# Kernel tuning notes

Hardware: AMD Instinct MI355X
Metric: run time of the kernel (lower is better)

Reference implementation:

```python
import jax, jax.numpy as jnp
import numpy as np

B, K, C, O, I = 32, 1024, 64, 32, 32  # batch, num_capsules, num_classes, out_dim, in_dim
NUM_ROUTING = 3


def squash(x, axis=-1):
    sq = jnp.sum(x * x, axis=axis, keepdims=True)
    return (sq / (1.0 + sq)) * x / jnp.sqrt(sq + 1e-8)


def setup_inputs() -> dict:
    key = jax.random.key(0)
    kx, kw = jax.random.split(key)
    x = jax.random.normal(kx, (B, K, I), dtype=jnp.float32)
    W = jax.random.normal(kw, (K, C, O, I), dtype=jnp.float32) * 0.01
    return {"x": x, "W": W}


def reference(x, W):
    # u_hat[b,k,c,o] = sum_i W[k,c,o,i] * x[b,k,i]  (the torch repeat+matmul)
    u_hat = jnp.einsum('kcoi,bki->bkco', W, x)  # [B,K,C,O]
    b_ij = jnp.zeros((B, K, C, 1), dtype=x.dtype)
    c_ij = None
    v_j = None
    for i in range(NUM_ROUTING):
        c_ij = jax.nn.softmax(b_ij, axis=2)              # softmax over classes
        s_j = jnp.sum(c_ij * u_hat, axis=1, keepdims=True)  # [B,1,C,O]
        v_j = squash(s_j, axis=-1)
        if i < NUM_ROUTING - 1:
            agreement = jnp.sum(u_hat * v_j, axis=-1, keepdims=True)  # [B,K,C,1]
            b_ij = b_ij + agreement
    return v_j[:, 0], c_ij[..., 0]  # ([B,C,O], [B,K,C])
```

## Files before the change

kernel.cpp:

```cpp
#include <hip/hip_runtime.h>
#include <stdint.h>

#define Bb 32
#define Kk 1024
#define Cc 64
#define Oo 32
#define Ii 32

typedef __attribute__((ext_vector_type(8))) short bf16x8;
typedef __attribute__((ext_vector_type(4))) float f32x4;

__device__ __forceinline__ short f2bf(float f) {
    uint32_t u = __builtin_bit_cast(uint32_t, f);
    u += 0x7fffu + ((u >> 16) & 1u);
    return (short)(u >> 16);
}
__device__ __forceinline__ float bflo(uint32_t u) { return __builtin_bit_cast(float, u << 16); }
__device__ __forceinline__ float bfhi(uint32_t u) { return __builtin_bit_cast(float, u & 0xffff0000u); }
__device__ __forceinline__ uint32_t pk2(float a, float b) {
    return (uint32_t)(uint16_t)f2bf(a) | ((uint32_t)(uint16_t)f2bf(b) << 16);
}


__global__ __launch_bounds__(256) void k_uhat(const float* __restrict__ x,
                                              const float* __restrict__ W,
                                              uint32_t* __restrict__ uh) {
    const int k = blockIdx.x;
    const int lane = threadIdx.x & 63;
    const int wave = threadIdx.x >> 6;
    const int m = lane & 15;
    const int q = lane >> 4;

    bf16x8 bfrag[2];
#pragma unroll
    for (int nb = 0; nb < 2; ++nb) {
        const float* xp = x + (size_t)((nb * 16 + m) * Kk + k) * Ii + q * 8;
        f32x4 a = *(const f32x4*)xp;
        f32x4 b = *(const f32x4*)(xp + 4);
        bf16x8 t;
        t[0] = f2bf(a.x); t[1] = f2bf(a.y); t[2] = f2bf(a.z); t[3] = f2bf(a.w);
        t[4] = f2bf(b.x); t[5] = f2bf(b.y); t[6] = f2bf(b.z); t[7] = f2bf(b.w);
        bfrag[nb] = t;
    }

    for (int cc = 0; cc < 16; ++cc) {
        const int c = wave * 16 + cc;
        bf16x8 afrag[2];
#pragma unroll
        for (int mo = 0; mo < 2; ++mo) {
            const float* wp = W + (size_t)((k * Cc + c) * Oo + mo * 16 + m) * Ii + q * 8;
            f32x4 a = __builtin_nontemporal_load((const f32x4*)wp);
            f32x4 b = __builtin_nontemporal_load((const f32x4*)(wp + 4));
            bf16x8 t;
            t[0] = f2bf(a.x); t[1] = f2bf(a.y); t[2] = f2bf(a.z); t[3] = f2bf(a.w);
            t[4] = f2bf(b.x); t[5] = f2bf(b.y); t[6] = f2bf(b.z); t[7] = f2bf(b.w);
            afrag[mo] = t;
        }
        const f32x4 z = {0.f, 0.f, 0.f, 0.f};
        f32x4 d0 = __builtin_amdgcn_mfma_f32_16x16x32_bf16(afrag[0], bfrag[0], z, 0, 0, 0);
        f32x4 d1 = __builtin_amdgcn_mfma_f32_16x16x32_bf16(afrag[0], bfrag[1], z, 0, 0, 0);
        f32x4 d2 = __builtin_amdgcn_mfma_f32_16x16x32_bf16(afrag[1], bfrag[0], z, 0, 0, 0);
        f32x4 d3 = __builtin_amdgcn_mfma_f32_16x16x32_bf16(afrag[1], bfrag[1], z, 0, 0, 0);

        uint4 p0, p1;
        p0.x = pk2(d0.x, d0.y); p0.y = pk2(d0.z, d0.w);
        p0.z = pk2(d1.x, d1.y); p0.w = pk2(d1.z, d1.w);
        p1.x = pk2(d2.x, d2.y); p1.y = pk2(d2.z, d2.w);
        p1.z = pk2(d3.x, d3.y); p1.w = pk2(d3.z, d3.w);
        uint32_t* dst = uh + (size_t)(k * Cc + c) * 512 + lane * 4;
        *(uint4*)dst = p0;
        *(uint4*)(dst + 256) = p1;
    }
}

template <bool UNIFORM>
__global__ __launch_bounds__(256) void k_sacc(const uint32_t* __restrict__ uh,
                                              const float* __restrict__ cij,
                                              float* __restrict__ part) {
    const int lane = threadIdx.x & 63;
    const int wave = threadIdx.x >> 6;
    const int m = lane & 15;
    const int c = (blockIdx.x & 15) * 4 + wave;
    const int chunk = blockIdx.x >> 4;
    const int k0 = chunk * 32;

    float acc[16];
#pragma unroll
    for (int i = 0; i < 16; ++i) acc[i] = 0.f;

    for (int kl = 0; kl < 32; ++kl) {
        const int k = k0 + kl;
        const uint32_t* up = uh + (size_t)(k * Cc + c) * 512 + lane * 4;
        uint4 q0 = *(const uint4*)up;
        uint4 q1 = *(const uint4*)(up + 256);
        float w0, w1;
        if (UNIFORM) {
            w0 = w1 = 1.0f / 64.0f;
        } else {
            const float* cp = cij + (size_t)(k * Cc + c) * Bb + m;
            w0 = cp[0];
            w1 = cp[16];
        }
        acc[0]  += w0 * bflo(q0.x);  acc[1]  += w0 * bfhi(q0.x);
        acc[2]  += w0 * bflo(q0.y);  acc[3]  += w0 * bfhi(q0.y);
        acc[4]  += w1 * bflo(q0.z);  acc[5]  += w1 * bfhi(q0.z);
        acc[6]  += w1 * bflo(q0.w);  acc[7]  += w1 * bfhi(q0.w);
        acc[8]  += w0 * bflo(q1.x);  acc[9]  += w0 * bfhi(q1.x);
        acc[10] += w0 * bflo(q1.y);  acc[11] += w0 * bfhi(q1.y);
        acc[12] += w1 * bflo(q1.z);  acc[13] += w1 * bfhi(q1.z);
        acc[14] += w1 * bflo(q1.w);  acc[15] += w1 * bfhi(q1.w);
    }
#pragma unroll
    for (int t = 0; t < 4; ++t) {
        f32x4 v = {acc[t * 4 + 0], acc[t * 4 + 1], acc[t * 4 + 2], acc[t * 4 + 3]};
        *(f32x4*)&part[(((size_t)(chunk * Cc + c) * 4 + t) * 64 + lane) * 4] = v;
    }
}

template <bool FINAL>
__global__ __launch_bounds__(256) void k_reduce(const float* __restrict__ part,
                                                float* __restrict__ vfrag,
                                                float* __restrict__ out_v) {
    __shared__ float red[4 * 64 * 17];
    const int c = blockIdx.x;
    const int tid = threadIdx.x;
    const int lane = tid & 63;
    const int cg = tid >> 6;

    float acc[16];
#pragma unroll
    for (int i = 0; i < 16; ++i) acc[i] = 0.f;
    for (int ch = cg * 8; ch < cg * 8 + 8; ++ch) {
        const f32x4* p = (const f32x4*)part + (size_t)(ch * Cc + c) * 4 * 64 + lane;
#pragma unroll
        for (int t = 0; t < 4; ++t) {
            f32x4 v = p[t * 64];
            acc[t * 4 + 0] += v.x; acc[t * 4 + 1] += v.y;
            acc[t * 4 + 2] += v.z; acc[t * 4 + 3] += v.w;
        }
    }
#pragma unroll
    for (int i = 0; i < 16; ++i) red[(cg * 64 + lane) * 17 + i] = acc[i];
    __syncthreads();

    if (tid < 64) {
        float a[16];
#pragma unroll
        for (int i = 0; i < 16; ++i)
            a[i] = red[tid * 17 + i] + red[(64 + tid) * 17 + i]
                 + red[(128 + tid) * 17 + i] + red[(192 + tid) * 17 + i];
        float sq0 = 0.f, sq1 = 0.f;
#pragma unroll
        for (int r = 0; r < 4; ++r) {
            sq0 += a[r] * a[r] + a[8 + r] * a[8 + r];
            sq1 += a[4 + r] * a[4 + r] + a[12 + r] * a[12 + r];
        }
        sq0 += __shfl_xor(sq0, 16); sq0 += __shfl_xor(sq0, 32);
        sq1 += __shfl_xor(sq1, 16); sq1 += __shfl_xor(sq1, 32);
        const float c0 = sq0 / ((1.f + sq0) * sqrtf(sq0 + 1e-8f));
        const float c1 = sq1 / ((1.f + sq1) * sqrtf(sq1 + 1e-8f));
#pragma unroll
        for (int r = 0; r < 4; ++r) {
            a[r] *= c0; a[8 + r] *= c0;
            a[4 + r] *= c1; a[12 + r] *= c1;
        }
        float* vp = vfrag + ((size_t)c * 64 + tid) * 16;
#pragma unroll
        for (int t = 0; t < 4; ++t) {
            f32x4 v = {a[t * 4 + 0], a[t * 4 + 1], a[t * 4 + 2], a[t * 4 + 3]};
            *(f32x4*)(vp + t * 4) = v;
        }
        if (FINAL) {
            const int m = tid & 15, q = tid >> 4;
#pragma unroll
            for (int t = 0; t < 4; ++t)
#pragma unroll
                for (int r = 0; r < 4; ++r) {
                    const int b = (t & 1) * 16 + m;
                    const int o = (t >> 1) * 16 + q * 4 + r;
                    out_v[((size_t)b * Cc + c) * Oo + o] = a[t * 4 + r];
                }
        }
    }
}

template <bool FIRST>
__global__ __launch_bounds__(256) void k_route(const uint32_t* __restrict__ uh,
                                               const float* __restrict__ vfrag,
                                               float* __restrict__ bbuf,
                                               float* __restrict__ cbuf,
                                               float* __restrict__ outc) {
    __shared__ float agr[4 * 64 * 32];
    const int tid = threadIdx.x;
    const int lane = tid & 63;
    const int wave = tid >> 6;
    const int m = lane & 15;
    const int q = lane >> 4;
    const int k0 = blockIdx.x * 4;

    for (int cc = 0; cc < 16; ++cc) {
        const int c = wave * 16 + cc;
        const float* vp = vfrag + ((size_t)c * 64 + lane) * 16;
        f32x4 vv[4];
#pragma unroll
        for (int t = 0; t < 4; ++t) vv[t] = *(const f32x4*)(vp + t * 4);
#pragma unroll
        for (int kl = 0; kl < 4; ++kl) {
            const int k = k0 + kl;
            const uint32_t* up = uh + (size_t)(k * Cc + c) * 512 + lane * 4;
            uint4 q0 = *(const uint4*)up;
            uint4 q1 = *(const uint4*)(up + 256);
            float p0 = bflo(q0.x) * vv[0].x + bfhi(q0.x) * vv[0].y
                     + bflo(q0.y) * vv[0].z + bfhi(q0.y) * vv[0].w
                     + bflo(q1.x) * vv[2].x + bfhi(q1.x) * vv[2].y
                     + bflo(q1.y) * vv[2].z + bfhi(q1.y) * vv[2].w;
            float p1 = bflo(q0.z) * vv[1].x + bfhi(q0.z) * vv[1].y
                     + bflo(q0.w) * vv[1].z + bfhi(q0.w) * vv[1].w
                     + bflo(q1.z) * vv[3].x + bfhi(q1.z) * vv[3].y
                     + bflo(q1.w) * vv[3].z + bfhi(q1.w) * vv[3].w;
            p0 += __shfl_xor(p0, 16);
            p0 += __shfl_xor(p0, 32);
            p1 += __shfl_xor(p1, 16);
            p1 += __shfl_xor(p1, 32);
            if (q == 0) {
                agr[(kl * 64 + c) * 32 + m] = p0;
                agr[(kl * 64 + c) * 32 + 16 + m] = p1;
            }
        }
    }
    __syncthreads();

    if (tid < 128) {
        const int kl = tid >> 5;
        const int b = tid & 31;
        const int k = k0 + kl;
        float row[64];
#pragma unroll
        for (int c = 0; c < 64; ++c) row[c] = agr[(kl * 64 + c) * 32 + b];
        if (FIRST) {
            float* bp = bbuf + (size_t)(k * Bb + b) * Cc;
#pragma unroll
            for (int c = 0; c < 64; ++c) bp[c] = row[c];
        } else {
            const float* bp = bbuf + (size_t)(k * Bb + b) * Cc;
#pragma unroll
            for (int c = 0; c < 64; ++c) row[c] += bp[c];
        }
        float mx = row[0];
#pragma unroll
        for (int c = 1; c < 64; ++c) mx = fmaxf(mx, row[c]);
        float sum = 0.f;
#pragma unroll
        for (int c = 0; c < 64; ++c) { row[c] = __expf(row[c] - mx); sum += row[c]; }
        const float inv = 1.f / sum;
#pragma unroll
        for (int c = 0; c < 64; ++c) row[c] *= inv;
        if (!FIRST) {
            float* op = outc + (size_t)(b * Kk + k) * Cc;
#pragma unroll
            for (int c = 0; c < 64; ++c) op[c] = row[c];
        }
#pragma unroll
        for (int c = 0; c < 64; ++c) agr[(kl * 64 + c) * 32 + b] = row[c];
    }
    __syncthreads();

    for (int idx = tid; idx < 4 * 64 * 32; idx += 256) {
        const int kl = idx >> 11;
        const int rem = idx & 2047;
        const int c = rem >> 5;
        const int b = rem & 31;
        cbuf[((size_t)(k0 + kl) * Cc + c) * Bb + b] = agr[idx];
    }
}

extern "C" void kernel_launch(void* const* d_in, const int* in_sizes, int n_in,
                              void* d_out, int out_size, void* d_ws, size_t ws_size,
                              hipStream_t stream) {
    (void)in_sizes; (void)n_in; (void)out_size;
    const float* x = (const float*)d_in[0];
    const float* W = (const float*)d_in[1];
    float* out_v = (float*)d_out;
    float* out_c = out_v + Bb * Cc * Oo;

    char* ws = (char*)d_ws;
    const size_t UH_BYTES = (size_t)Kk * Cc * 512 * 4;
    const size_t PART_BYTES = (size_t)32 * Cc * 4 * 64 * 4 * 4;
    const size_t BB_BYTES = (size_t)Kk * Bb * Cc * 4;
    const size_t VF_BYTES = (size_t)Cc * 64 * 16 * 4;

    uint32_t* uh = (uint32_t*)ws;
    float* part  = (float*)(ws + UH_BYTES);
    float* bbuf  = (float*)(ws + UH_BYTES + PART_BYTES);
    float* cbuf  = (float*)(ws + UH_BYTES + PART_BYTES + BB_BYTES);
    float* vfrag = (float*)(ws + UH_BYTES + PART_BYTES + 2 * BB_BYTES);
    const size_t NEED = UH_BYTES + PART_BYTES + 2 * BB_BYTES + VF_BYTES;
    if (ws_size < NEED) return;

    k_uhat<<<Kk, 256, 0, stream>>>(x, W, uh);
    k_sacc<true><<<512, 256, 0, stream>>>(uh, nullptr, part);
    k_reduce<false><<<Cc, 256, 0, stream>>>(part, vfrag, nullptr);
    k_route<true><<<256, 256, 0, stream>>>(uh, vfrag, bbuf, cbuf, nullptr);
    k_sacc<false><<<512, 256, 0, stream>>>(uh, cbuf, part);
    k_reduce<false><<<Cc, 256, 0, stream>>>(part, vfrag, nullptr);
    k_route<false><<<256, 256, 0, stream>>>(uh, vfrag, bbuf, cbuf, out_c);
    k_sacc<false><<<512, 256, 0, stream>>>(uh, cbuf, part);
    k_reduce<true><<<Cc, 256, 0, stream>>>(part, vfrag, out_v);
}
```

Measured before the change: 519.0 us.

## Fuse routing softmax with weighted s_j accumulation and split reduction in two stages

The routing kernel now also computes the c_ij-weighted partial sums of u_hat for its 4 capsules, reading the softmax weights from shared memory. This removes the cbuf round trip and the separate k_sacc pass over u_hat. Partials are stored as bf16 and reduced in two stages (k_red1 over 512 blocks, then k_red2 per class), which gives more parallelism than the old 64-block reduce. Blocks grow to 512 threads. The trade-off is extra precision loss from bf16 partials and more kernel launches.

```diff
diff --git a/kernel.cpp b/kernel.cpp
--- a/kernel.cpp
+++ b/kernel.cpp
@@ -73,13 +73,10 @@
     }
 }
 
-template <bool UNIFORM>
-__global__ __launch_bounds__(256) void k_sacc(const uint32_t* __restrict__ uh,
-                                              const float* __restrict__ cij,
-                                              float* __restrict__ part) {
+__global__ __launch_bounds__(256) void k_sacc0(const uint32_t* __restrict__ uh,
+                                               float* __restrict__ part0) {
     const int lane = threadIdx.x & 63;
     const int wave = threadIdx.x >> 6;
-    const int m = lane & 15;
     const int c = (blockIdx.x & 15) * 4 + wave;
     const int chunk = blockIdx.x >> 4;
     const int k0 = chunk * 32;
@@ -89,38 +86,28 @@
     for (int i = 0; i < 16; ++i) acc[i] = 0.f;
 
     for (int kl = 0; kl < 32; ++kl) {
-        const int k = k0 + kl;
-        const uint32_t* up = uh + (size_t)(k * Cc + c) * 512 + lane * 4;
+        const uint32_t* up = uh + (size_t)((k0 + kl) * Cc + c) * 512 + lane * 4;
         uint4 q0 = *(const uint4*)up;
         uint4 q1 = *(const uint4*)(up + 256);
-        float w0, w1;
-        if (UNIFORM) {
-            w0 = w1 = 1.0f / 64.0f;
-        } else {
-            const float* cp = cij + (size_t)(k * Cc + c) * Bb + m;
-            w0 = cp[0];
-            w1 = cp[16];
-        }
+        const float w0 = 1.0f / 64.0f;
         acc[0]  += w0 * bflo(q0.x);  acc[1]  += w0 * bfhi(q0.x);
         acc[2]  += w0 * bflo(q0.y);  acc[3]  += w0 * bfhi(q0.y);
-        acc[4]  += w1 * bflo(q0.z);  acc[5]  += w1 * bfhi(q0.z);
-        acc[6]  += w1 * bflo(q0.w);  acc[7]  += w1 * bfhi(q0.w);
+        acc[4]  += w0 * bflo(q0.z);  acc[5]  += w0 * bfhi(q0.z);
+        acc[6]  += w0 * bflo(q0.w);  acc[7]  += w0 * bfhi(q0.w);
         acc[8]  += w0 * bflo(q1.x);  acc[9]  += w0 * bfhi(q1.x);
         acc[10] += w0 * bflo(q1.y);  acc[11] += w0 * bfhi(q1.y);
-        acc[12] += w1 * bflo(q1.z);  acc[13] += w1 * bfhi(q1.z);
-        acc[14] += w1 * bflo(q1.w);  acc[15] += w1 * bfhi(q1.w);
+        acc[12] += w0 * bflo(q1.z);  acc[13] += w0 * bfhi(q1.z);
+        acc[14] += w0 * bflo(q1.w);  acc[15] += w0 * bfhi(q1.w);
     }
 #pragma unroll
     for (int t = 0; t < 4; ++t) {
         f32x4 v = {acc[t * 4 + 0], acc[t * 4 + 1], acc[t * 4 + 2], acc[t * 4 + 3]};
-        *(f32x4*)&part[(((size_t)(chunk * Cc + c) * 4 + t) * 64 + lane) * 4] = v;
-    }
-}
-
-template <bool FINAL>
-__global__ __launch_bounds__(256) void k_reduce(const float* __restrict__ part,
-                                                float* __restrict__ vfrag,
-                                                float* __restrict__ out_v) {
+        *(f32x4*)&part0[(((size_t)(chunk * Cc + c) * 4 + t) * 64 + lane) * 4] = v;
+    }
+}
+
+__global__ __launch_bounds__(256) void k_reduce0(const float* __restrict__ part0,
+                                                 float* __restrict__ vfrag) {
     __shared__ float red[4 * 64 * 17];
     const int c = blockIdx.x;
     const int tid = threadIdx.x;
@@ -131,7 +118,7 @@
 #pragma unroll
     for (int i = 0; i < 16; ++i) acc[i] = 0.f;
     for (int ch = cg * 8; ch < cg * 8 + 8; ++ch) {
-        const f32x4* p = (const f32x4*)part + (size_t)(ch * Cc + c) * 4 * 64 + lane;
+        const f32x4* p = (const f32x4*)part0 + (size_t)(ch * Cc + c) * 4 * 64 + lane;
 #pragma unroll
         for (int t = 0; t < 4; ++t) {
             f32x4 v = p[t * 64];
@@ -170,54 +157,43 @@
             f32x4 v = {a[t * 4 + 0], a[t * 4 + 1], a[t * 4 + 2], a[t * 4 + 3]};
             *(f32x4*)(vp + t * 4) = v;
         }
-        if (FINAL) {
-            const int m = tid & 15, q = tid >> 4;
-#pragma unroll
-            for (int t = 0; t < 4; ++t)
-#pragma unroll
-                for (int r = 0; r < 4; ++r) {
-                    const int b = (t & 1) * 16 + m;
-                    const int o = (t >> 1) * 16 + q * 4 + r;
-                    out_v[((size_t)b * Cc + c) * Oo + o] = a[t * 4 + r];
-                }
-        }
-    }
-}
-
-template <bool FIRST>
-__global__ __launch_bounds__(256) void k_route(const uint32_t* __restrict__ uh,
-                                               const float* __restrict__ vfrag,
-                                               float* __restrict__ bbuf,
-                                               float* __restrict__ cbuf,
-                                               float* __restrict__ outc) {
+    }
+}
+
+template <bool FINAL>
+__global__ __launch_bounds__(512) void k_iter(const uint32_t* __restrict__ uh,
+                                              const float* __restrict__ vfrag,
+                                              float* __restrict__ bbuf,
+                                              uint32_t* __restrict__ partB,
+                                              float* __restrict__ outc) {
     __shared__ float agr[4 * 64 * 32];
     const int tid = threadIdx.x;
     const int lane = tid & 63;
-    const int wave = tid >> 6;
+    const int w = tid >> 6;
     const int m = lane & 15;
     const int q = lane >> 4;
     const int k0 = blockIdx.x * 4;
 
-    for (int cc = 0; cc < 16; ++cc) {
-        const int c = wave * 16 + cc;
+    for (int cc = 0; cc < 8; ++cc) {
+        const int c = w * 8 + cc;
         const float* vp = vfrag + ((size_t)c * 64 + lane) * 16;
-        f32x4 vv[4];
-#pragma unroll
-        for (int t = 0; t < 4; ++t) vv[t] = *(const f32x4*)(vp + t * 4);
+        f32x4 vv0 = *(const f32x4*)(vp);
+        f32x4 vv1 = *(const f32x4*)(vp + 4);
+        f32x4 vv2 = *(const f32x4*)(vp + 8);
+        f32x4 vv3 = *(const f32x4*)(vp + 12);
 #pragma unroll
         for (int kl = 0; kl < 4; ++kl) {
-            const int k = k0 + kl;
-            const uint32_t* up = uh + (size_t)(k * Cc + c) * 512 + lane * 4;
+            const uint32_t* up = uh + (size_t)((k0 + kl) * Cc + c) * 512 + lane * 4;
             uint4 q0 = *(const uint4*)up;
             uint4 q1 = *(const uint4*)(up + 256);
-            float p0 = bflo(q0.x) * vv[0].x + bfhi(q0.x) * vv[0].y
-                     + bflo(q0.y) * vv[0].z + bfhi(q0.y) * vv[0].w
-                     + bflo(q1.x) * vv[2].x + bfhi(q1.x) * vv[2].y
-                     + bflo(q1.y) * vv[2].z + bfhi(q1.y) * vv[2].w;
-            float p1 = bflo(q0.z) * vv[1].x + bfhi(q0.z) * vv[1].y
-                     + bflo(q0.w) * vv[1].z + bfhi(q0.w) * vv[1].w
-                     + bflo(q1.z) * vv[3].x + bfhi(q1.z) * vv[3].y
-                     + bflo(q1.w) * vv[3].z + bfhi(q1.w) * vv[3].w;
+            float p0 = bflo(q0.x) * vv0.x + bfhi(q0.x) * vv0.y
+                     + bflo(q0.y) * vv0.z + bfhi(q0.y) * vv0.w
+                     + bflo(q1.x) * vv2.x + bfhi(q1.x) * vv2.y
+                     + bflo(q1.y) * vv2.z + bfhi(q1.y) * vv2.w;
+            float p1 = bflo(q0.z) * vv1.x + bfhi(q0.z) * vv1.y
+                     + bflo(q0.w) * vv1.z + bfhi(q0.w) * vv1.w
+                     + bflo(q1.z) * vv3.x + bfhi(q1.z) * vv3.y
+                     + bflo(q1.w) * vv3.z + bfhi(q1.w) * vv3.w;
             p0 += __shfl_xor(p0, 16);
             p0 += __shfl_xor(p0, 32);
             p1 += __shfl_xor(p1, 16);
@@ -237,7 +213,7 @@
         float row[64];
 #pragma unroll
         for (int c = 0; c < 64; ++c) row[c] = agr[(kl * 64 + c) * 32 + b];
-        if (FIRST) {
+        if (!FINAL) {
             float* bp = bbuf + (size_t)(k * Bb + b) * Cc;
 #pragma unroll
             for (int c = 0; c < 64; ++c) bp[c] = row[c];
@@ -255,7 +231,7 @@
         const float inv = 1.f / sum;
 #pragma unroll
         for (int c = 0; c < 64; ++c) row[c] *= inv;
-        if (!FIRST) {
+        if (FINAL) {
             float* op = outc + (size_t)(b * Kk + k) * Cc;
 #pragma unroll
             for (int c = 0; c < 64; ++c) op[c] = row[c];
@@ -265,12 +241,135 @@
     }
     __syncthreads();
 
-    for (int idx = tid; idx < 4 * 64 * 32; idx += 256) {
-        const int kl = idx >> 11;
-        const int rem = idx & 2047;
-        const int c = rem >> 5;
-        const int b = rem & 31;
-        cbuf[((size_t)(k0 + kl) * Cc + c) * Bb + b] = agr[idx];
+    const int chunk = blockIdx.x;
+    for (int cg = 0; cg < 8; ++cg) {
+        const int c = w * 8 + cg;
+        float acc[16];
+#pragma unroll
+        for (int i = 0; i < 16; ++i) acc[i] = 0.f;
+#pragma unroll
+        for (int kl = 0; kl < 4; ++kl) {
+            const uint32_t* up = uh + (size_t)((k0 + kl) * Cc + c) * 512 + lane * 4;
+            uint4 q0 = *(const uint4*)up;
+            uint4 q1 = *(const uint4*)(up + 256);
+            const float w0 = agr[(kl * 64 + c) * 32 + m];
+            const float w1 = agr[(kl * 64 + c) * 32 + 16 + m];
+            acc[0]  += w0 * bflo(q0.x);  acc[1]  += w0 * bfhi(q0.x);
+            acc[2]  += w0 * bflo(q0.y);  acc[3]  += w0 * bfhi(q0.y);
+            acc[4]  += w1 * bflo(q0.z);  acc[5]  += w1 * bfhi(q0.z);
+            acc[6]  += w1 * bflo(q0.w);  acc[7]  += w1 * bfhi(q0.w);
+            acc[8]  += w0 * bflo(q1.x);  acc[9]  += w0 * bfhi(q1.x);
+            acc[10] += w0 * bflo(q1.y);  acc[11] += w0 * bfhi(q1.y);
+            acc[12] += w1 * bflo(q1.z);  acc[13] += w1 * bfhi(q1.z);
+            acc[14] += w1 * bflo(q1.w);  acc[15] += w1 * bfhi(q1.w);
+        }
+        uint4 o0, o1;
+        o0.x = pk2(acc[0],  acc[1]);  o0.y = pk2(acc[2],  acc[3]);
+        o0.z = pk2(acc[4],  acc[5]);  o0.w = pk2(acc[6],  acc[7]);
+        o1.x = pk2(acc[8],  acc[9]);  o1.y = pk2(acc[10], acc[11]);
+        o1.z = pk2(acc[12], acc[13]); o1.w = pk2(acc[14], acc[15]);
+        uint32_t* dst = partB + ((size_t)(c * 256 + chunk) * 64 + lane) * 8;
+        *(uint4*)dst = o0;
+        *(uint4*)(dst + 4) = o1;
+    }
+}
+
+__global__ __launch_bounds__(256) void k_red1(const uint32_t* __restrict__ partB,
+                                              float* __restrict__ part2) {
+    __shared__ float red[4 * 64 * 17];
+    const int cb = blockIdx.x;
+    const int c = cb >> 3;
+    const int g = cb & 7;
+    const int tid = threadIdx.x;
+    const int lane = tid & 63;
+    const int ww = tid >> 6;
+
+    float acc[16];
+#pragma unroll
+    for (int i = 0; i < 16; ++i) acc[i] = 0.f;
+    for (int ch = g * 32 + ww * 8; ch < g * 32 + ww * 8 + 8; ++ch) {
+        const uint32_t* p = partB + ((size_t)(c * 256 + ch) * 64 + lane) * 8;
+        uint4 a = *(const uint4*)p;
+        uint4 b = *(const uint4*)(p + 4);
+        acc[0]  += bflo(a.x);  acc[1]  += bfhi(a.x);
+        acc[2]  += bflo(a.y);  acc[3]  += bfhi(a.y);
+        acc[4]  += bflo(a.z);  acc[5]  += bfhi(a.z);
+        acc[6]  += bflo(a.w);  acc[7]  += bfhi(a.w);
+        acc[8]  += bflo(b.x);  acc[9]  += bfhi(b.x);
+        acc[10] += bflo(b.y);  acc[11] += bfhi(b.y);
+        acc[12] += bflo(b.z);  acc[13] += bfhi(b.z);
+        acc[14] += bflo(b.w);  acc[15] += bfhi(b.w);
+    }
+#pragma unroll
+    for (int i = 0; i < 16; ++i) red[(ww * 64 + lane) * 17 + i] = acc[i];
+    __syncthreads();
+
+    if (tid < 64) {
+        float a[16];
+#pragma unroll
+        for (int i = 0; i < 16; ++i)
+            a[i] = red[tid * 17 + i] + red[(64 + tid) * 17 + i]
+                 + red[(128 + tid) * 17 + i] + red[(192 + tid) * 17 + i];
+        float* dst = part2 + ((size_t)cb * 64 + tid) * 16;
+#pragma unroll
+        for (int t = 0; t < 4; ++t) {
+            f32x4 v = {a[t * 4 + 0], a[t * 4 + 1], a[t * 4 + 2], a[t * 4 + 3]};
+            *(f32x4*)(dst + t * 4) = v;
+        }
+    }
+}
+
+template <bool FINAL>
+__global__ __launch_bounds__(64) void k_red2(const float* __restrict__ part2,
+                                             float* __restrict__ vfrag,
+                                             float* __restrict__ out_v) {
+    const int c = blockIdx.x;
+    const int lane = threadIdx.x;
+    const int m = lane & 15;
+    const int q = lane >> 4;
+
+    float a[16];
+#pragma unroll
+    for (int i = 0; i < 16; ++i) a[i] = 0.f;
+    for (int g = 0; g < 8; ++g) {
+        const float* p = part2 + ((size_t)(c * 8 + g) * 64 + lane) * 16;
+#pragma unroll
+        for (int t = 0; t < 4; ++t) {
+            f32x4 v = *(const f32x4*)(p + t * 4);
+            a[t * 4 + 0] += v.x; a[t * 4 + 1] += v.y;
+            a[t * 4 + 2] += v.z; a[t * 4 + 3] += v.w;
+        }
+    }
+    float sq0 = 0.f, sq1 = 0.f;
+#pragma unroll
+    for (int r = 0; r < 4; ++r) {
+        sq0 += a[r] * a[r] + a[8 + r] * a[8 + r];
+        sq1 += a[4 + r] * a[4 + r] + a[12 + r] * a[12 + r];
+    }
+    sq0 += __shfl_xor(sq0, 16); sq0 += __shfl_xor(sq0, 32);
+    sq1 += __shfl_xor(sq1, 16); sq1 += __shfl_xor(sq1, 32);
+    const float c0 = sq0 / ((1.f + sq0) * sqrtf(sq0 + 1e-8f));
+    const float c1 = sq1 / ((1.f + sq1) * sqrtf(sq1 + 1e-8f));
+#pragma unroll
+    for (int r = 0; r < 4; ++r) {
+        a[r] *= c0; a[8 + r] *= c0;
+        a[4 + r] *= c1; a[12 + r] *= c1;
+    }
+    float* vp = vfrag + ((size_t)c * 64 + lane) * 16;
+#pragma unroll
+    for (int t = 0; t < 4; ++t) {
+        f32x4 v = {a[t * 4 + 0], a[t * 4 + 1], a[t * 4 + 2], a[t * 4 + 3]};
+        *(f32x4*)(vp + t * 4) = v;
+    }
+    if (FINAL) {
+#pragma unroll
+        for (int t = 0; t < 4; ++t)
+#pragma unroll
+            for (int r = 0; r < 4; ++r) {
+                const int b = (t & 1) * 16 + m;
+                const int o = (t >> 1) * 16 + q * 4 + r;
+                out_v[((size_t)b * Cc + c) * Oo + o] = a[t * 4 + r];
+            }
     }
 }
 
@@ -285,25 +384,28 @@
 
     char* ws = (char*)d_ws;
     const size_t UH_BYTES = (size_t)Kk * Cc * 512 * 4;
-    const size_t PART_BYTES = (size_t)32 * Cc * 4 * 64 * 4 * 4;
+    const size_t P0_BYTES = (size_t)32 * Cc * 4 * 64 * 4 * 4;
+    const size_t PB_BYTES = (size_t)Cc * 256 * 64 * 8 * 4;
+    const size_t P2_BYTES = (size_t)512 * 64 * 16 * 4;
     const size_t BB_BYTES = (size_t)Kk * Bb * Cc * 4;
     const size_t VF_BYTES = (size_t)Cc * 64 * 16 * 4;
 
-    uint32_t* uh = (uint32_t*)ws;
-    float* part  = (float*)(ws + UH_BYTES);
-    float* bbuf  = (float*)(ws + UH_BYTES + PART_BYTES);
-    float* cbuf  = (float*)(ws + UH_BYTES + PART_BYTES + BB_BYTES);
-    float* vfrag = (float*)(ws + UH_BYTES + PART_BYTES + 2 * BB_BYTES);
-    const size_t NEED = UH_BYTES + PART_BYTES + 2 * BB_BYTES + VF_BYTES;
+    uint32_t* uh = (uint32_t*)ws;                      ws += UH_BYTES;
+    float* part0  = (float*)ws;                        ws += P0_BYTES;
+    uint32_t* partB = (uint32_t*)ws;                   ws += PB_BYTES;
+    float* part2  = (float*)ws;                        ws += P2_BYTES;
+    float* bbuf   = (float*)ws;                        ws += BB_BYTES;
+    float* vfrag  = (float*)ws;                        ws += VF_BYTES;
+    const size_t NEED = UH_BYTES + P0_BYTES + PB_BYTES + P2_BYTES + BB_BYTES + VF_BYTES;
     if (ws_size < NEED) return;
 
     k_uhat<<<Kk, 256, 0, stream>>>(x, W, uh);
-    k_sacc<true><<<512, 256, 0, stream>>>(uh, nullptr, part);
-    k_reduce<false><<<Cc, 256, 0, stream>>>(part, vfrag, nullptr);
-    k_route<true><<<256, 256, 0, stream>>>(uh, vfrag, bbuf, cbuf, nullptr);
-    k_sacc<false><<<512, 256, 0, stream>>>(uh, cbuf, part);
-    k_reduce<false><<<Cc, 256, 0, stream>>>(part, vfrag, nullptr);
-    k_route<false><<<256, 256, 0, stream>>>(uh, vfrag, bbuf, cbuf, out_c);
-    k_sacc<false><<<512, 256, 0, stream>>>(uh, cbuf, part);
-    k_reduce<true><<<Cc, 256, 0, stream>>>(part, vfrag, out_v);
-}
+    k_sacc0<<<512, 256, 0, stream>>>(uh, part0);
+    k_reduce0<<<Cc, 256, 0, stream>>>(part0, vfrag);
+    k_iter<false><<<256, 512, 0, stream>>>(uh, vfrag, bbuf, partB, nullptr);
+    k_red1<<<512, 256, 0, stream>>>(partB, part2);
+    k_red2<false><<<Cc, 64, 0, stream>>>(part2, vfrag, nullptr);
+    k_iter<true><<<256, 512, 0, stream>>>(uh, vfrag, bbuf, partB, out_c);
+    k_red1<<<512, 256, 0, stream>>>(partB, part2);
+    k_red2<true><<<Cc, 64, 0, stream>>>(part2, vfrag, out_v);
+}
```

New measurement: 526.0 us. About the same (+1.4%).
